# Optimization experiments

Measured on AMD Instinct MI355X. Metric: run time of the kernel, lower is better.

## Reference

```python
import jax, jax.numpy as jnp
import numpy as np

HID = 768
NSPLITS = 12
HEAD_RATIO = 2
H = NSPLITS // HEAD_RATIO          # 6 attention heads
D = HID // NSPLITS                 # 64 head size
AH = H * D                         # 384 all_head_size
KS = 9                             # conv kernel size
PAD = (KS - 1) // 2
B, S = 4, 1024


def setup_inputs() -> dict:
    key = jax.random.key(0)
    ks = jax.random.split(key, 16)
    std = 0.02
    inp = {
        "Q": jax.random.normal(ks[0], (B, S, HID), jnp.float32),
        "K": jax.random.normal(ks[1], (B, S, HID), jnp.float32),
        "V": jax.random.normal(ks[2], (B, S, HID), jnp.float32),
        "td": jax.random.uniform(ks[3], (B, S), jnp.float32),
        "mask": jax.random.randint(ks[4], (B, S), 0, 2, jnp.int32),
        # projection weights, applied as x @ W (in, out)
        "Wq": jax.random.normal(ks[5], (HID, AH), jnp.float32) * std,
        "Wk": jax.random.normal(ks[6], (HID, AH), jnp.float32) * std,
        "Wv": jax.random.normal(ks[7], (HID, AH), jnp.float32) * std,
        # separable conv: depthwise (HID, KS), pointwise (AH, HID), bias (AH,)
        "dw_w": jax.random.normal(ks[8], (HID, KS), jnp.float32) * std,
        "pw_w": jax.random.normal(ks[9], (AH, HID), jnp.float32) * std,
        "sep_b": jnp.zeros((AH,), jnp.float32),
        # conv_kernel_layer Linear(AH -> H*KS)
        "ck_W": jax.random.normal(ks[10], (AH, H * KS), jnp.float32) * std,
        "ck_b": jnp.zeros((H * KS,), jnp.float32),
        # conv_out_layer Linear(HID -> AH)
        "co_W": jax.random.normal(ks[11], (HID, AH), jnp.float32) * std,
        "co_b": jnp.zeros((AH,), jnp.float32),
        # gammas init to zeros as in torch module
        "gammas": jnp.zeros((H, 1, 1), jnp.float32),
    }
    return inp


def dist_func(scores, td, am, gammas):
    # scores: [B,H,S,S]; am: [B,1,1,S] bool key mask; entirely non-differentiable.
    s = scores.shape[-1]
    dt = scores.dtype
    amf = am.astype(dt)
    p = jax.nn.softmax(jnp.where(am, scores, -1e8), axis=-1) * amf
    distcum = jnp.cumsum(p, axis=-1)
    disttotal = jnp.sum(p, axis=-1, keepdims=True)
    # |j - i| position distance
    pos = jnp.abs(jnp.arange(s)[None, :] - jnp.arange(s)[:, None]).astype(dt)
    dist_scores = jnp.sqrt(jnp.clip((disttotal - distcum) * pos[None, None], 0.0, None))
    gamma = -jax.nn.softplus(gammas)[None]  # (1,H,1,1)
    total_effect = jnp.clip(jnp.exp(dist_scores * gamma), 1e-5, 1e5)
    # time-distance effect on strictly-lower-triangular positions
    tdn = td / jnp.maximum(jnp.linalg.norm(td, axis=-1, keepdims=True), 1e-12)
    td_scores = jnp.broadcast_to(tdn[:, None, None, :], scores.shape)
    td_sm = jax.nn.softmax(jnp.where(am, td_scores, -1e4), axis=-1)
    lower = jnp.tril(jnp.ones((s, s), dt), -1)  # (triu == 0)
    return jax.lax.stop_gradient(total_effect - td_sm * lower[None, None])


def reference(Q, K, V, td, mask, Wq, Wk, Wv, dw_w, pw_w, sep_b, ck_W, ck_b, co_W, co_b, gammas):
    b, s, hid = Q.shape
    mq = Q @ Wq  # (B,S,AH)
    mk = K @ Wk
    mv = V @ Wv
    # SeparableConv1D over sequence dim of K
    x = jnp.transpose(K, (0, 2, 1))  # (B,HID,S)
    dw = jax.lax.conv_general_dilated(
        x, dw_w[:, None, :], window_strides=(1,), padding=[(PAD, PAD)],
        feature_group_count=hid, dimension_numbers=("NCH", "OIH", "NCH"))
    pw = jnp.einsum("bcs,oc->bos", dw, pw_w) + sep_b[None, :, None]
    mkc = jnp.transpose(pw, (0, 2, 1))  # (B,S,AH)

    q = mq.reshape(b, s, H, D).transpose(0, 2, 1, 3)
    k = mk.reshape(b, s, H, D).transpose(0, 2, 1, 3)
    v = mv.reshape(b, s, H, D).transpose(0, 2, 1, 3)

    # dynamic span convolution
    conv_attn = mkc * mq                                   # (B,S,AH)
    ck = (conv_attn @ ck_W + ck_b).reshape(b, s, H, KS)
    ck = jax.nn.softmax(ck, axis=-1)                       # per-position kernel
    co = V @ co_W + co_b                                   # (B,S,AH)
    co_pad = jnp.pad(co, ((0, 0), (PAD, PAD), (0, 0)))
    idx = jnp.arange(s)[:, None] + jnp.arange(KS)[None, :]  # (S,KS)
    unf = co_pad[:, idx, :].reshape(b, s, KS, H, D)         # sliding window gather
    conv_out = jnp.einsum("bskhd,bshk->bshd", unf, ck)      # (B,S,H,D)

    # attention with distance decay
    scores = jnp.einsum("bhid,bhjd->bhij", q, k) / np.float32(np.sqrt(D))
    am = (mask[:, None, None, :] != 0)  # (B,1,1,S) key mask
    total_effect = dist_func(scores, td, am, gammas)
    scores = jnp.where(am, scores * total_effect, -1e8)
    probs = jax.nn.softmax(scores, axis=-1)
    ctx = jnp.einsum("bhij,bhjd->bhid", probs, v).transpose(0, 2, 1, 3)  # (B,S,H,D)

    out = jnp.concatenate([ctx, conv_out], axis=2).reshape(b, s, HEAD_RATIO * AH)
    return out
```

## Files before the change

### kernel.cpp

```cpp
#include <hip/hip_runtime.h>
#include <hip/hip_bf16.h>

#define HIDC 768
#define Hh   6
#define Dd   64
#define AHc  384
#define KSc  9
#define PADc 4
#define Bb   4
#define Ss   1024
#define MRr  (Bb * Ss)

typedef __attribute__((ext_vector_type(8))) __bf16 bf16x8;
typedef __attribute__((ext_vector_type(4))) __bf16 bf16x4;
typedef __attribute__((ext_vector_type(4))) float  f32x4;

__device__ __forceinline__ void gl_lds16(const void* g, void* l) {
    __builtin_amdgcn_global_load_lds(
        (const __attribute__((address_space(1))) void*)g,
        (__attribute__((address_space(3))) void*)l, 16, 0, 0);
}

__device__ __forceinline__ void split8(const float* p, bf16x8& hi, bf16x8& lo) {
    float4 x0 = *(const float4*)p;
    float4 x1 = *(const float4*)(p + 4);
    float xs[8] = {x0.x, x0.y, x0.z, x0.w, x1.x, x1.y, x1.z, x1.w};
#pragma unroll
    for (int e = 0; e < 8; ++e) {
        __bf16 hv = (__bf16)xs[e];
        hi[e] = hv;
        lo[e] = (__bf16)(xs[e] - (float)hv);
    }
}

__device__ __forceinline__ void split8r(const float* xs, bf16x8& hi, bf16x8& lo) {
#pragma unroll
    for (int e = 0; e < 8; ++e) {
        __bf16 hv = (__bf16)xs[e];
        hi[e] = hv;
        lo[e] = (__bf16)(xs[e] - (float)hv);
    }
}

__device__ __forceinline__ bf16x8 cvt8(const float* p) {
    float4 x0 = *(const float4*)p;
    float4 x1 = *(const float4*)(p + 4);
    float xs[8] = {x0.x, x0.y, x0.z, x0.w, x1.x, x1.y, x1.z, x1.w};
    bf16x8 h;
#pragma unroll
    for (int e = 0; e < 8; ++e) h[e] = (__bf16)xs[e];
    return h;
}

__global__ __launch_bounds__(256) void k_pre(
        const float* __restrict__ Wq, const float* __restrict__ Wk,
        const float* __restrict__ Wv, const float* __restrict__ coW,
        const float* __restrict__ pww, const float* __restrict__ cob,
        const float* __restrict__ sepb, const float* __restrict__ td,
        const int* __restrict__ mask, const float* __restrict__ Kin,
        const float* __restrict__ dww, const float* __restrict__ Q,
        const float* __restrict__ V,
        __bf16* __restrict__ Whi, __bf16* __restrict__ Wlo,
        float* __restrict__ biasb, float* __restrict__ td_sm,
        __bf16* __restrict__ dwbf, __bf16* __restrict__ qbf,
        __bf16* __restrict__ vbf) {
    __shared__ float shmem[64 * 65];
    int bid = blockIdx.x;
    int tid = threadIdx.x;
    if (bid < 288) {
        int z = bid / 72, rem = bid % 72;
        int n0 = (rem % 6) * 64, k0 = (rem / 6) * 64;
        const float* src = (z == 0) ? Wq : (z == 1) ? Wk : (z == 2) ? Wv : coW;
        float (*tile)[65] = (float(*)[65])shmem;
        int r = tid >> 2, cq = tid & 3;
#pragma unroll
        for (int e = 0; e < 4; ++e) {
            float4 v = *(const float4*)&src[(size_t)(k0 + r) * AHc + n0 + cq * 16 + e * 4];
            tile[r][cq * 16 + e * 4 + 0] = v.x;
            tile[r][cq * 16 + e * 4 + 1] = v.y;
            tile[r][cq * 16 + e * 4 + 2] = v.z;
            tile[r][cq * 16 + e * 4 + 3] = v.w;
        }
        __syncthreads();
        float x[16];
#pragma unroll
        for (int e = 0; e < 16; ++e) x[e] = tile[cq * 16 + e][r];
        bf16x8 h0, l0, h1, l1;
        split8r(x, h0, l0);
        split8r(x + 8, h1, l1);
        size_t dst = ((size_t)(z * AHc + n0 + r)) * HIDC + k0 + cq * 16;
        *(bf16x8*)(Whi + dst)     = h0;
        *(bf16x8*)(Whi + dst + 8) = h1;
        *(bf16x8*)(Wlo + dst)     = l0;
        *(bf16x8*)(Wlo + dst + 8) = l1;
        return;
    }
    if (bid < 432) {
        int idx = (bid - 288) * 256 + tid;
        bf16x8 hi, lo;
        split8(pww + (size_t)idx * 8, hi, lo);
        size_t dst = (size_t)4 * AHc * HIDC + (size_t)idx * 8;
        *(bf16x8*)(Whi + dst) = hi;
        *(bf16x8*)(Wlo + dst) = lo;
        return;
    }
    if (bid < 440) {
        int idx = (bid - 432) * 256 + tid;
        if (idx < 5 * AHc) {
            int z = idx / AHc, n = idx % AHc;
            biasb[idx] = (z == 3) ? cob[n] : (z == 4) ? sepb[n] : 0.f;
        }
        return;
    }
    if (bid < 444) {
        int b = bid - 440;
        float* red = shmem;
        float* tv  = shmem + 256;
        float ls = 0.f;
        for (int j = tid; j < Ss; j += 256) {
            float v = td[b * Ss + j];
            tv[j] = v;
            ls += v * v;
        }
        red[tid] = ls; __syncthreads();
        for (int s = 128; s > 0; s >>= 1) { if (tid < s) red[tid] += red[tid + s]; __syncthreads(); }
        float norm = fmaxf(sqrtf(red[0]), 1e-12f);
        __syncthreads();
        float lm = -3e38f;
        for (int j = tid; j < Ss; j += 256) {
            float v = mask[b * Ss + j] ? tv[j] / norm : -1e4f;
            tv[j] = v;
            lm = fmaxf(lm, v);
        }
        red[tid] = lm; __syncthreads();
        for (int s = 128; s > 0; s >>= 1) { if (tid < s) red[tid] = fmaxf(red[tid], red[tid + s]); __syncthreads(); }
        float m = red[0]; __syncthreads();
        float lsum = 0.f;
        for (int j = tid; j < Ss; j += 256) {
            float e = expf(tv[j] - m);
            tv[j] = e;
            lsum += e;
        }
        red[tid] = lsum; __syncthreads();
        for (int s = 128; s > 0; s >>= 1) { if (tid < s) red[tid] += red[tid + s]; __syncthreads(); }
        float inv = 1.f / red[0];
        __syncthreads();
        for (int j = tid; j < Ss; j += 256)
            td_sm[b * Ss + j] = tv[j] * inv;
        return;
    }
    int db = bid - 444;
    if (db < 3072) {
        int idx = db * 256 + tid;
        int c4 = idx % (HIDC / 4);
        int s  = (idx / (HIDC / 4)) % Ss;
        int b  = idx / ((HIDC / 4) * Ss);
        int c  = c4 * 4;
        float wv[4][KSc];
#pragma unroll
        for (int j = 0; j < 4; ++j)
#pragma unroll
            for (int k = 0; k < KSc; ++k) wv[j][k] = dww[(c + j) * KSc + k];
        float4 acc = {0.f, 0.f, 0.f, 0.f};
#pragma unroll
        for (int k = 0; k < KSc; ++k) {
            int sp = s + k - PADc;
            if (sp >= 0 && sp < Ss) {
                float4 v = *(const float4*)&Kin[(size_t)(b * Ss + sp) * HIDC + c];
                acc.x += v.x * wv[0][k]; acc.y += v.y * wv[1][k];
                acc.z += v.z * wv[2][k]; acc.w += v.w * wv[3][k];
            }
        }
        bf16x4 o = {(__bf16)acc.x, (__bf16)acc.y, (__bf16)acc.z, (__bf16)acc.w};
        *(bf16x4*)(dwbf + (size_t)idx * 4) = o;
    } else {
        const int n8 = MRr * HIDC / 8;
        int idx = (db - 3072) * 256 + tid;
        if (idx < n8) {
            *(bf16x8*)(qbf + (size_t)idx * 8) = cvt8(Q + (size_t)idx * 8);
        } else {
            int i = idx - n8;
            *(bf16x8*)(vbf + (size_t)i * 8) = cvt8(V + (size_t)i * 8);
        }
    }
}

__global__ __launch_bounds__(256) void k_gemm5(
        const __bf16* __restrict__ qbf, const float* __restrict__ Kin,
        const __bf16* __restrict__ vbf, const __bf16* __restrict__ dwbf,
        const __bf16* __restrict__ Whi, const __bf16* __restrict__ Wlo,
        const float* __restrict__ biasb, float* __restrict__ Call,
        __bf16* __restrict__ kh, __bf16* __restrict__ kl,
        __bf16* __restrict__ qh, __bf16* __restrict__ vt) {
    __shared__ __attribute__((aligned(16))) __bf16 As [128 * 32];
    __shared__ __attribute__((aligned(16))) __bf16 BsH[128 * 32];
    __shared__ __attribute__((aligned(16))) __bf16 BsL[128 * 32];

    int wg = blockIdx.x + 3 * (blockIdx.y + 32 * blockIdx.z);
    int n2 = (wg & 7) * 60 + (wg >> 3);
    int bxx = n2 % 3, byy = (n2 / 3) % 32, z = n2 / 96;

    int m0 = byy * 128, n0 = bxx * 128;
    int tid = threadIdx.x;
    int wave = tid >> 6, lane = tid & 63, quad = lane >> 4, l15 = lane & 15;

    int lrow = lane >> 2;
    int lswz = 8 * ((lane & 3) ^ (lrow & 3));

    int brow = wave * 32 + lrow;
    const __bf16* BhG0 = Whi + ((size_t)(z * AHc + n0 + brow)) * HIDC + lswz;
    const __bf16* BhG1 = BhG0 + (size_t)16 * HIDC;
    const __bf16* BlG0 = Wlo + ((size_t)(z * AHc + n0 + brow)) * HIDC + lswz;
    const __bf16* BlG1 = BlG0 + (size_t)16 * HIDC;
    __bf16* BhL0 = BsH + (wave * 2 + 0) * 512;
    __bf16* BhL1 = BsH + (wave * 2 + 1) * 512;
    __bf16* BlL0 = BsL + (wave * 2 + 0) * 512;
    __bf16* BlL1 = BsL + (wave * 2 + 1) * 512;

    const __bf16* Abf = (z == 0) ? qbf : (z == 4) ? dwbf : vbf;
    const __bf16* AG0 = Abf + ((size_t)(m0 + wave * 32 + lrow)) * HIDC + lswz;
    const __bf16* AG1 = AG0 + (size_t)16 * HIDC;
    __bf16* AL0 = As + (wave * 2 + 0) * 512;
    __bf16* AL1 = As + (wave * 2 + 1) * 512;

    int sr = tid >> 1;
    int sk = (tid & 1) * 16;
    const float* Arow = Kin + (size_t)(m0 + sr) * HIDC + sk;
    int g0 = sk >> 3;
    int d0 = sr * 32 + ((g0       ^ (sr & 3)) * 8);
    int d1 = sr * 32 + (((g0 + 1) ^ (sr & 3)) * 8);

    int swz = (quad ^ (l15 & 3)) * 8;
    f32x4 acc[4][4] = {};

    for (int k0 = 0; k0 < HIDC; k0 += 32) {
        if (z == 1) {
            const float* ap = Arow + k0;
            *(bf16x8*)&As[d0] = cvt8(ap);
            *(bf16x8*)&As[d1] = cvt8(ap + 8);
        } else {
            gl_lds16(AG0 + k0, AL0);
            gl_lds16(AG1 + k0, AL1);
        }
        gl_lds16(BhG0 + k0, BhL0);
        gl_lds16(BhG1 + k0, BhL1);
        gl_lds16(BlG0 + k0, BlL0);
        gl_lds16(BlG1 + k0, BlL1);
        __syncthreads();

        int mrow = (wave >> 1) * 64 + l15;
        int nrow = (wave & 1) * 64 + l15;
        bf16x8 ah[4], bh[4], bl[4];
#pragma unroll
        for (int mt = 0; mt < 4; ++mt)
            ah[mt] = *(bf16x8*)&As[(mrow + mt * 16) * 32 + swz];
#pragma unroll
        for (int nt = 0; nt < 4; ++nt) {
            bh[nt] = *(bf16x8*)&BsH[(nrow + nt * 16) * 32 + swz];
            bl[nt] = *(bf16x8*)&BsL[(nrow + nt * 16) * 32 + swz];
        }
#pragma unroll
        for (int mt = 0; mt < 4; ++mt)
#pragma unroll
            for (int nt = 0; nt < 4; ++nt) {
                acc[mt][nt] = __builtin_amdgcn_mfma_f32_16x16x32_bf16(ah[mt], bh[nt], acc[mt][nt], 0, 0, 0);
                acc[mt][nt] = __builtin_amdgcn_mfma_f32_16x16x32_bf16(ah[mt], bl[nt], acc[mt][nt], 0, 0, 0);
            }
        __syncthreads();
    }

    if (z == 1) {
#pragma unroll
        for (int nt = 0; nt < 4; ++nt) {
            int n = n0 + (wave & 1) * 64 + nt * 16 + l15;
#pragma unroll
            for (int mt = 0; mt < 4; ++mt) {
#pragma unroll
                for (int r = 0; r < 4; ++r) {
                    int m = m0 + (wave >> 1) * 64 + mt * 16 + quad * 4 + r;
                    float v = acc[mt][nt][r];
                    __bf16 hv = (__bf16)v;
                    kh[(size_t)m * AHc + n] = hv;
                    kl[(size_t)m * AHc + n] = (__bf16)(v - (float)hv);
                }
            }
        }
    } else if (z == 2) {
        int b = m0 >> 10;
#pragma unroll
        for (int nt = 0; nt < 4; ++nt) {
            int n = (wave & 1) * 64 + nt * 16 + l15;
            int gn = n0 + n;
            int h = gn >> 6, d = gn & 63;
#pragma unroll
            for (int mt = 0; mt < 4; ++mt) {
                int m = m0 + (wave >> 1) * 64 + mt * 16 + quad * 4;
                int s = m & (Ss - 1);
                bf16x4 o = {(__bf16)acc[mt][nt][0], (__bf16)acc[mt][nt][1],
                            (__bf16)acc[mt][nt][2], (__bf16)acc[mt][nt][3]};
                *(bf16x4*)&vt[((size_t)((b * Hh + h) * Dd + d)) * Ss + s] = o;
            }
        }
    } else if (z == 0) {
#pragma unroll
        for (int nt = 0; nt < 4; ++nt) {
            int n = n0 + (wave & 1) * 64 + nt * 16 + l15;
#pragma unroll
            for (int mt = 0; mt < 4; ++mt) {
#pragma unroll
                for (int r = 0; r < 4; ++r) {
                    int m = m0 + (wave >> 1) * 64 + mt * 16 + quad * 4 + r;
                    float v = acc[mt][nt][r];
                    Call[(size_t)m * AHc + n] = v;
                    qh[(size_t)m * AHc + n] = (__bf16)v;
                }
            }
        }
    } else {
        float* Cz = Call + (size_t)z * MRr * AHc;
        const float* bz = biasb + z * AHc;
#pragma unroll
        for (int nt = 0; nt < 4; ++nt) {
            int n = n0 + (wave & 1) * 64 + nt * 16 + l15;
            float bias = bz[n];
#pragma unroll
            for (int mt = 0; mt < 4; ++mt) {
#pragma unroll
                for (int r = 0; r < 4; ++r) {
                    int m = m0 + (wave >> 1) * 64 + mt * 16 + quad * 4 + r;
                    Cz[(size_t)m * AHc + n] = acc[mt][nt][r] + bias;
                }
            }
        }
    }
}

__global__ __launch_bounds__(256) void k_ckconv(const float* __restrict__ mkc,
                                                const float* __restrict__ mq,
                                                const float* __restrict__ ckW,
                                                const float* __restrict__ ckb,
                                                const float* __restrict__ co,
                                                float* __restrict__ out) {
    int tid = threadIdx.x;
    int lr = tid >> 6, lane = tid & 63;
    int row = blockIdx.x * 4 + lr;
    __shared__ float ca[4][AHc];
    __shared__ float ckv[4][Hh * KSc];
    for (int o = lane; o < AHc; o += 64)
        ca[lr][o] = mkc[(size_t)row * AHc + o] * mq[(size_t)row * AHc + o];
    __syncthreads();
    if (lane < Hh * KSc) {
        float acc = ckb[lane];
        for (int o = 0; o < AHc; ++o)
            acc += ca[lr][o] * ckW[o * (Hh * KSc) + lane];
        ckv[lr][lane] = acc;
    }
    __syncthreads();
    if (lane < Hh) {
        float m = -3e38f;
#pragma unroll
        for (int k = 0; k < KSc; ++k) m = fmaxf(m, ckv[lr][lane * KSc + k]);
        float e[KSc];
        float s = 0.f;
#pragma unroll
        for (int k = 0; k < KSc; ++k) { e[k] = expf(ckv[lr][lane * KSc + k] - m); s += e[k]; }
        float inv = 1.f / s;
#pragma unroll
        for (int k = 0; k < KSc; ++k) ckv[lr][lane * KSc + k] = e[k] * inv;
    }
    __syncthreads();
#pragma unroll
    for (int e = 0; e < 2; ++e) {
        int it = e * 256 + tid;
        if (it >= 4 * (AHc / 4)) break;
        int r4i = it / (AHc / 4), dq = it % (AHc / 4);
        int h = dq >> 4, d4 = dq & 15;
        int row2 = blockIdx.x * 4 + r4i;
        int s = row2 & (Ss - 1), b = row2 >> 10;
        float4 acc = {0.f, 0.f, 0.f, 0.f};
#pragma unroll
        for (int k = 0; k < KSc; ++k) {
            int sp = s + k - PADc;
            if (sp >= 0 && sp < Ss) {
                float4 v = *(const float4*)&co[(size_t)(b * Ss + sp) * AHc + h * Dd + d4 * 4];
                float wv = ckv[r4i][h * KSc + k];
                acc.x += wv * v.x; acc.y += wv * v.y; acc.z += wv * v.z; acc.w += wv * v.w;
            }
        }
        *(float4*)&out[(size_t)row2 * (2 * AHc) + AHc + h * Dd + d4 * 4] = acc;
    }
}

__device__ __forceinline__ int scix(int m, int j) {
    return m * 1024 + (j ^ (((m ^ (j >> 6)) & 7) << 2));
}

__global__ __launch_bounds__(512, 4) void k_attn(const __bf16* __restrict__ qh,
                                              const __bf16* __restrict__ kh, const __bf16* __restrict__ kl,
                                              const __bf16* __restrict__ vt,
                                              const int* __restrict__ mask,
                                              const float* __restrict__ td_sm, const float* __restrict__ gammas,
                                              float* __restrict__ out) {
    __shared__ float sc[16 * 1024];
    int wg = blockIdx.x + 64 * blockIdx.y;
    int n  = (wg & 7) * 192 + (wg >> 3);
    int bx = n & 63, by = n >> 6;
    int i0 = bx * 16;
    int h = by % Hh, b = by / Hh;
    int tid = threadIdx.x;
    int w = tid >> 6, lane = tid & 63, quad = lane >> 4, l15 = lane & 15;
    int jw = w * 128;

    bf16x8 a_hi[2];
    {
        size_t qoff = (size_t)(b * Ss + i0 + l15) * AHc + h * Dd + quad * 8;
        a_hi[0] = *(const bf16x8*)(qh + qoff);
        a_hi[1] = *(const bf16x8*)(qh + qoff + 32);
    }
#pragma unroll 4
    for (int t = 0; t < 8; ++t) {
        int jt = jw + t * 16;
        size_t koff = (size_t)(b * Ss + jt + l15) * AHc + h * Dd + quad * 8;
        f32x4 acc = {0.f, 0.f, 0.f, 0.f};
#pragma unroll
        for (int kc = 0; kc < 2; ++kc) {
            bf16x8 khv = *(const bf16x8*)(kh + koff + kc * 32);
            bf16x8 klv = *(const bf16x8*)(kl + koff + kc * 32);
            acc = __builtin_amdgcn_mfma_f32_16x16x32_bf16(a_hi[kc], khv, acc, 0, 0, 0);
            acc = __builtin_amdgcn_mfma_f32_16x16x32_bf16(a_hi[kc], klv, acc, 0, 0, 0);
        }
#pragma unroll
        for (int r = 0; r < 4; ++r)
            sc[scix(quad * 4 + r, jt + l15)] = acc[r] * 0.125f;
    }
    __syncthreads();

    const int* mrow = mask + b * Ss;
    const float* tdrow = td_sm + b * Ss;
    float gamma = -log1pf(expf(gammas[h]));
    int jb = lane << 4;
    __attribute__((aligned(16))) int marr[16];
    {
        const int4* mp = (const int4*)(mrow + jb);
#pragma unroll
        for (int k = 0; k < 4; ++k) ((int4*)marr)[k] = mp[k];
    }
    __attribute__((aligned(16))) float tdv[16];
    {
        const float4* tp = (const float4*)(tdrow + jb);
#pragma unroll
        for (int k = 0; k < 4; ++k) ((float4*)tdv)[k] = tp[k];
    }

    {
        int mA = w * 2, mB = mA + 1;
        int iA = i0 + mA, iB = i0 + mB;
        __attribute__((aligned(16))) float sA[16], sB[16];
        float pA[16], pB[16];
#pragma unroll
        for (int g = 0; g < 4; ++g) {
            *(f32x4*)(sA + 4 * g) = *(const f32x4*)&sc[scix(mA, jb + 4 * g)];
            *(f32x4*)(sB + 4 * g) = *(const f32x4*)&sc[scix(mB, jb + 4 * g)];
        }
        float mxA = -1e30f, mxB = -1e30f;
#pragma unroll
        for (int jj = 0; jj < 16; ++jj) {
            mxA = fmaxf(mxA, marr[jj] ? sA[jj] : -1e30f);
            mxB = fmaxf(mxB, marr[jj] ? sB[jj] : -1e30f);
        }
#pragma unroll
        for (int d = 1; d < 64; d <<= 1) {
            mxA = fmaxf(mxA, __shfl_xor(mxA, d));
            mxB = fmaxf(mxB, __shfl_xor(mxB, d));
        }
#pragma unroll
        for (int jj = 0; jj < 16; ++jj) {
            pA[jj] = marr[jj] ? __expf(sA[jj] - mxA) : 0.f;
            pB[jj] = marr[jj] ? __expf(sB[jj] - mxB) : 0.f;
        }
#pragma unroll
        for (int jj = 1; jj < 16; ++jj) { pA[jj] += pA[jj - 1]; pB[jj] += pB[jj - 1]; }
        float tA = pA[15], tB = pB[15];
        float incA = tA, incB = tB;
#pragma unroll
        for (int dlt = 1; dlt < 64; dlt <<= 1) {
            float vA = __shfl_up(incA, dlt);
            float vB = __shfl_up(incB, dlt);
            if (lane >= dlt) { incA += vA; incB += vB; }
        }
        float offA = incA - tA, offB = incB - tB;
        float totA = __shfl(incA, 63), totB = __shfl(incB, 63);
        float invA = 1.f / fmaxf(totA, 1e-30f), invB = 1.f / fmaxf(totB, 1e-30f);
        float mx2A = -1e30f, mx2B = -1e30f;
#pragma unroll
        for (int jj = 0; jj < 16; ++jj) {
            int j = jb + jj;
            float cumA = pA[jj] + offA, cumB = pB[jj] + offB;
            float posA = fabsf((float)(j - iA));
            float posB = fabsf((float)(j - iB));
            float dsA = sqrtf(fmaxf((totA - cumA) * invA * posA, 0.f));
            float dsB = sqrtf(fmaxf((totB - cumB) * invB * posB, 0.f));
            float teA = fminf(fmaxf(__expf(dsA * gamma), 1e-5f), 1e5f);
            float teB = fminf(fmaxf(__expf(dsB * gamma), 1e-5f), 1e5f);
            float tdj = tdv[jj];
            float multA = teA - ((j < iA) ? tdj : 0.f);
            float multB = teB - ((j < iB) ? tdj : 0.f);
            float s2A = marr[jj] ? sA[jj] * multA : -1e8f;
            float s2B = marr[jj] ? sB[jj] * multB : -1e8f;
            sA[jj] = s2A; sB[jj] = s2B;
            mx2A = fmaxf(mx2A, s2A); mx2B = fmaxf(mx2B, s2B);
        }
#pragma unroll
        for (int d = 1; d < 64; d <<= 1) {
            mx2A = fmaxf(mx2A, __shfl_xor(mx2A, d));
            mx2B = fmaxf(mx2B, __shfl_xor(mx2B, d));
        }
        float smA = 0.f, smB = 0.f;
#pragma unroll
        for (int jj = 0; jj < 16; ++jj) {
            sA[jj] = __expf(sA[jj] - mx2A); smA += sA[jj];
            sB[jj] = __expf(sB[jj] - mx2B); smB += sB[jj];
        }
#pragma unroll
        for (int d = 1; d < 64; d <<= 1) {
            smA += __shfl_xor(smA, d);
            smB += __shfl_xor(smB, d);
        }
        float i2A = 1.f / smA, i2B = 1.f / smB;
#pragma unroll
        for (int jj = 0; jj < 16; ++jj) { sA[jj] *= i2A; sB[jj] *= i2B; }
#pragma unroll
        for (int g = 0; g < 4; ++g) {
            *(f32x4*)&sc[scix(mA, jb + 4 * g)] = *(const f32x4*)(sA + 4 * g);
            *(f32x4*)&sc[scix(mB, jb + 4 * g)] = *(const f32x4*)(sB + 4 * g);
        }
    }
    __syncthreads();

    f32x4 oacc[4] = {};
    const __bf16* vtb = vt + (size_t)(b * Hh + h) * Dd * Ss;
#pragma unroll
    for (int kc = 0; kc < 4; ++kc) {
        int j0 = jw + kc * 32 + quad * 8;
        __attribute__((aligned(16))) float x[8];
        *(f32x4*)x       = *(const f32x4*)&sc[scix(l15, j0)];
        *(f32x4*)(x + 4) = *(const f32x4*)&sc[scix(l15, j0 + 4)];
        bf16x8 p_hi, p_lo;
        split8r(x, p_hi, p_lo);
#pragma unroll
        for (int nt = 0; nt < 4; ++nt) {
            int d = nt * 16 + l15;
            bf16x8 vv = *(const bf16x8*)(vtb + (size_t)d * Ss + j0);
            oacc[nt] = __builtin_amdgcn_mfma_f32_16x16x32_bf16(p_hi, vv, oacc[nt], 0, 0, 0);
            oacc[nt] = __builtin_amdgcn_mfma_f32_16x16x32_bf16(p_lo, vv, oacc[nt], 0, 0, 0);
        }
    }
    __syncthreads();
#pragma unroll
    for (int nt = 0; nt < 4; ++nt)
#pragma unroll
        for (int r = 0; r < 4; ++r)
            sc[w * 1024 + (quad * 4 + r) * 64 + nt * 16 + l15] = oacc[nt][r];
    __syncthreads();
#pragma unroll
    for (int e = 0; e < 2; ++e) {
        int idx = e * 512 + tid;
        int m = idx >> 6, dd = idx & 63;
        float v = 0.f;
#pragma unroll
        for (int ww = 0; ww < 8; ++ww) v += sc[ww * 1024 + idx];
        out[(size_t)(b * Ss + i0 + m) * (2 * AHc) + h * Dd + dd] = v;
    }
}

extern "C" void kernel_launch(void* const* d_in, const int* in_sizes, int n_in,
                              void* d_out, int out_size, void* d_ws, size_t ws_size,
                              hipStream_t stream) {
    const float* Q    = (const float*)d_in[0];
    const float* Kin  = (const float*)d_in[1];
    const float* V    = (const float*)d_in[2];
    const float* td   = (const float*)d_in[3];
    const int*   mask = (const int*)d_in[4];
    const float* Wq   = (const float*)d_in[5];
    const float* Wk   = (const float*)d_in[6];
    const float* Wv   = (const float*)d_in[7];
    const float* dww  = (const float*)d_in[8];
    const float* pww  = (const float*)d_in[9];
    const float* sepb = (const float*)d_in[10];
    const float* ckW  = (const float*)d_in[11];
    const float* ckb  = (const float*)d_in[12];
    const float* coW  = (const float*)d_in[13];
    const float* cob  = (const float*)d_in[14];
    const float* gam  = (const float*)d_in[15];
    float* out = (float*)d_out;
    float* ws = (float*)d_ws;

    float* mq    = ws;
    float* mks   = mq    + (size_t)MRr * AHc;
    float* mvs   = mks   + (size_t)MRr * AHc;
    float* co    = mvs   + (size_t)MRr * AHc;
    float* mkc   = co    + (size_t)MRr * AHc;
    float* dwr   = mkc   + (size_t)MRr * AHc;
    float* tdsm  = dwr   + (size_t)MRr * HIDC;
    float* biasb = tdsm  + (size_t)Bb * Ss;

    __bf16* dwbf = (__bf16*)dwr;
    __bf16* qbf  = (__bf16*)(dwr + (size_t)MRr * HIDC / 2);
    __bf16* kh = (__bf16*)mks;
    __bf16* kl = kh + (size_t)MRr * AHc;
    __bf16* vt = (__bf16*)mvs;
    __bf16* qh = vt + (size_t)MRr * AHc;

    __bf16* Whi = (__bf16*)d_out;
    __bf16* Wlo = Whi + (size_t)5 * AHc * HIDC;
    __bf16* vbf = Wlo + (size_t)5 * AHc * HIDC;

    k_pre<<<6588, 256, 0, stream>>>(Wq, Wk, Wv, coW, pww, cob, sepb, td, mask,
                                    Kin, dww, Q, V, Whi, Wlo, biasb, tdsm,
                                    dwbf, qbf, vbf);

    dim3 gg(AHc / 128, MRr / 128, 5);
    k_gemm5<<<gg, 256, 0, stream>>>(qbf, Kin, vbf, dwbf, Whi, Wlo, biasb, mq, kh, kl, qh, vt);

    k_ckconv<<<MRr / 4, 256, 0, stream>>>(mkc, mq, ckW, ckb, co, out);

    dim3 ga(Ss / 16, Bb * Hh);
    k_attn<<<ga, 512, 0, stream>>>(qh, kh, kl, vt, mask, tdsm, gam, out);
}
```

Measured before the change: 272.6 us.

## Double-buffer GEMM LDS tiles, pack attention mask bits, tweak ckconv and attn bounds

The projection GEMM now keeps two LDS tile buffers and issues the global-to-LDS loads for the next K slice before computing the current one, so load latency can overlap the MFMA work. In the attention kernel the per-lane mask is packed into a 16-bit integer rather than a 16-int array, and masked scores are set to a sentinel before the max and exp steps. This is meant to cut register pressure and the number of selects. The ckconv inner loop gets an unrolled strided weight pointer, and the attention launch bounds are given as explicit AMDGPU attributes. Doubling the GEMM's LDS use may reduce occupancy, and exp of the -1e30 sentinel must underflow to zero to keep the masked probabilities correct.

```diff
diff --git a/kernel.cpp b/kernel.cpp
--- a/kernel.cpp
+++ b/kernel.cpp
@@ -192,9 +192,9 @@
         const float* __restrict__ biasb, float* __restrict__ Call,
         __bf16* __restrict__ kh, __bf16* __restrict__ kl,
         __bf16* __restrict__ qh, __bf16* __restrict__ vt) {
-    __shared__ __attribute__((aligned(16))) __bf16 As [128 * 32];
-    __shared__ __attribute__((aligned(16))) __bf16 BsH[128 * 32];
-    __shared__ __attribute__((aligned(16))) __bf16 BsL[128 * 32];
+    __shared__ __attribute__((aligned(16))) __bf16 As [2][128 * 32];
+    __shared__ __attribute__((aligned(16))) __bf16 BsH[2][128 * 32];
+    __shared__ __attribute__((aligned(16))) __bf16 BsL[2][128 * 32];
 
     int wg = blockIdx.x + 3 * (blockIdx.y + 32 * blockIdx.z);
     int n2 = (wg & 7) * 60 + (wg >> 3);
@@ -206,22 +206,19 @@
 
     int lrow = lane >> 2;
     int lswz = 8 * ((lane & 3) ^ (lrow & 3));
+
+    int off0 = (wave * 2 + 0) * 512;
+    int off1 = (wave * 2 + 1) * 512;
 
     int brow = wave * 32 + lrow;
     const __bf16* BhG0 = Whi + ((size_t)(z * AHc + n0 + brow)) * HIDC + lswz;
     const __bf16* BhG1 = BhG0 + (size_t)16 * HIDC;
     const __bf16* BlG0 = Wlo + ((size_t)(z * AHc + n0 + brow)) * HIDC + lswz;
     const __bf16* BlG1 = BlG0 + (size_t)16 * HIDC;
-    __bf16* BhL0 = BsH + (wave * 2 + 0) * 512;
-    __bf16* BhL1 = BsH + (wave * 2 + 1) * 512;
-    __bf16* BlL0 = BsL + (wave * 2 + 0) * 512;
-    __bf16* BlL1 = BsL + (wave * 2 + 1) * 512;
 
     const __bf16* Abf = (z == 0) ? qbf : (z == 4) ? dwbf : vbf;
     const __bf16* AG0 = Abf + ((size_t)(m0 + wave * 32 + lrow)) * HIDC + lswz;
     const __bf16* AG1 = AG0 + (size_t)16 * HIDC;
-    __bf16* AL0 = As + (wave * 2 + 0) * 512;
-    __bf16* AL1 = As + (wave * 2 + 1) * 512;
 
     int sr = tid >> 1;
     int sk = (tid & 1) * 16;
@@ -231,33 +228,50 @@
     int d1 = sr * 32 + (((g0 + 1) ^ (sr & 3)) * 8);
 
     int swz = (quad ^ (l15 & 3)) * 8;
+    int mrow = (wave >> 1) * 64 + l15;
+    int nrow = (wave & 1) * 64 + l15;
     f32x4 acc[4][4] = {};
 
-    for (int k0 = 0; k0 < HIDC; k0 += 32) {
-        if (z == 1) {
-            const float* ap = Arow + k0;
-            *(bf16x8*)&As[d0] = cvt8(ap);
-            *(bf16x8*)&As[d1] = cvt8(ap + 8);
-        } else {
-            gl_lds16(AG0 + k0, AL0);
-            gl_lds16(AG1 + k0, AL1);
-        }
-        gl_lds16(BhG0 + k0, BhL0);
-        gl_lds16(BhG1 + k0, BhL1);
-        gl_lds16(BlG0 + k0, BlL0);
-        gl_lds16(BlG1 + k0, BlL1);
-        __syncthreads();
-
-        int mrow = (wave >> 1) * 64 + l15;
-        int nrow = (wave & 1) * 64 + l15;
+    if (z == 1) {
+        *(bf16x8*)&As[0][d0] = cvt8(Arow);
+        *(bf16x8*)&As[0][d1] = cvt8(Arow + 8);
+    } else {
+        gl_lds16(AG0, &As[0][off0]);
+        gl_lds16(AG1, &As[0][off1]);
+    }
+    gl_lds16(BhG0, &BsH[0][off0]);
+    gl_lds16(BhG1, &BsH[0][off1]);
+    gl_lds16(BlG0, &BsL[0][off0]);
+    gl_lds16(BlG1, &BsL[0][off1]);
+    __syncthreads();
+
+    int cur = 0;
+    for (int t = 0; t < HIDC / 32; ++t) {
+        int nxt = cur ^ 1;
+        if (t + 1 < HIDC / 32) {
+            int k1 = (t + 1) * 32;
+            if (z == 1) {
+                const float* ap = Arow + k1;
+                *(bf16x8*)&As[nxt][d0] = cvt8(ap);
+                *(bf16x8*)&As[nxt][d1] = cvt8(ap + 8);
+            } else {
+                gl_lds16(AG0 + k1, &As[nxt][off0]);
+                gl_lds16(AG1 + k1, &As[nxt][off1]);
+            }
+            gl_lds16(BhG0 + k1, &BsH[nxt][off0]);
+            gl_lds16(BhG1 + k1, &BsH[nxt][off1]);
+            gl_lds16(BlG0 + k1, &BsL[nxt][off0]);
+            gl_lds16(BlG1 + k1, &BsL[nxt][off1]);
+        }
+
         bf16x8 ah[4], bh[4], bl[4];
 #pragma unroll
         for (int mt = 0; mt < 4; ++mt)
-            ah[mt] = *(bf16x8*)&As[(mrow + mt * 16) * 32 + swz];
+            ah[mt] = *(bf16x8*)&As[cur][(mrow + mt * 16) * 32 + swz];
 #pragma unroll
         for (int nt = 0; nt < 4; ++nt) {
-            bh[nt] = *(bf16x8*)&BsH[(nrow + nt * 16) * 32 + swz];
-            bl[nt] = *(bf16x8*)&BsL[(nrow + nt * 16) * 32 + swz];
+            bh[nt] = *(bf16x8*)&BsH[cur][(nrow + nt * 16) * 32 + swz];
+            bl[nt] = *(bf16x8*)&BsL[cur][(nrow + nt * 16) * 32 + swz];
         }
 #pragma unroll
         for (int mt = 0; mt < 4; ++mt)
@@ -267,6 +281,7 @@
                 acc[mt][nt] = __builtin_amdgcn_mfma_f32_16x16x32_bf16(ah[mt], bl[nt], acc[mt][nt], 0, 0, 0);
             }
         __syncthreads();
+        cur = nxt;
     }
 
     if (z == 1) {
@@ -351,8 +366,10 @@
     __syncthreads();
     if (lane < Hh * KSc) {
         float acc = ckb[lane];
+        const float* wp = ckW + lane;
+#pragma unroll 8
         for (int o = 0; o < AHc; ++o)
-            acc += ca[lr][o] * ckW[o * (Hh * KSc) + lane];
+            acc += ca[lr][o] * wp[o * (Hh * KSc)];
         ckv[lr][lane] = acc;
     }
     __syncthreads();
@@ -395,12 +412,13 @@
     return m * 1024 + (j ^ (((m ^ (j >> 6)) & 7) << 2));
 }
 
-__global__ __launch_bounds__(512, 4) void k_attn(const __bf16* __restrict__ qh,
-                                              const __bf16* __restrict__ kh, const __bf16* __restrict__ kl,
-                                              const __bf16* __restrict__ vt,
-                                              const int* __restrict__ mask,
-                                              const float* __restrict__ td_sm, const float* __restrict__ gammas,
-                                              float* __restrict__ out) {
+__global__ __attribute__((amdgpu_flat_work_group_size(512, 512), amdgpu_waves_per_eu(4, 4)))
+void k_attn(const __bf16* __restrict__ qh,
+            const __bf16* __restrict__ kh, const __bf16* __restrict__ kl,
+            const __bf16* __restrict__ vt,
+            const int* __restrict__ mask,
+            const float* __restrict__ td_sm, const float* __restrict__ gammas,
+            float* __restrict__ out) {
     __shared__ float sc[16 * 1024];
     int wg = blockIdx.x + 64 * blockIdx.y;
     int n  = (wg & 7) * 192 + (wg >> 3);
@@ -435,15 +453,20 @@
     }
     __syncthreads();
 
-    const int* mrow = mask + b * Ss;
     const float* tdrow = td_sm + b * Ss;
     float gamma = -log1pf(expf(gammas[h]));
     int jb = lane << 4;
-    __attribute__((aligned(16))) int marr[16];
+    int mbits = 0;
     {
-        const int4* mp = (const int4*)(mrow + jb);
-#pragma unroll
-        for (int k = 0; k < 4; ++k) ((int4*)marr)[k] = mp[k];
+        const int4* mp = (const int4*)(mask + b * Ss + jb);
+#pragma unroll
+        for (int k = 0; k < 4; ++k) {
+            int4 mv = mp[k];
+            mbits |= (mv.x != 0) << (4 * k + 0);
+            mbits |= (mv.y != 0) << (4 * k + 1);
+            mbits |= (mv.z != 0) << (4 * k + 2);
+            mbits |= (mv.w != 0) << (4 * k + 3);
+        }
     }
     __attribute__((aligned(16))) float tdv[16];
     {
@@ -462,11 +485,15 @@
             *(f32x4*)(sA + 4 * g) = *(const f32x4*)&sc[scix(mA, jb + 4 * g)];
             *(f32x4*)(sB + 4 * g) = *(const f32x4*)&sc[scix(mB, jb + 4 * g)];
         }
+#pragma unroll
+        for (int jj = 0; jj < 16; ++jj) {
+            if (!((mbits >> jj) & 1)) { sA[jj] = -1e30f; sB[jj] = -1e30f; }
+        }
         float mxA = -1e30f, mxB = -1e30f;
 #pragma unroll
         for (int jj = 0; jj < 16; ++jj) {
-            mxA = fmaxf(mxA, marr[jj] ? sA[jj] : -1e30f);
-            mxB = fmaxf(mxB, marr[jj] ? sB[jj] : -1e30f);
+            mxA = fmaxf(mxA, sA[jj]);
+            mxB = fmaxf(mxB, sB[jj]);
         }
 #pragma unroll
         for (int d = 1; d < 64; d <<= 1) {
@@ -475,8 +502,8 @@
         }
 #pragma unroll
         for (int jj = 0; jj < 16; ++jj) {
-            pA[jj] = marr[jj] ? __expf(sA[jj] - mxA) : 0.f;
-            pB[jj] = marr[jj] ? __expf(sB[jj] - mxB) : 0.f;
+            pA[jj] = __expf(sA[jj] - mxA);
+            pB[jj] = __expf(sB[jj] - mxB);
         }
 #pragma unroll
         for (int jj = 1; jj < 16; ++jj) { pA[jj] += pA[jj - 1]; pB[jj] += pB[jj - 1]; }
@@ -495,6 +522,7 @@
 #pragma unroll
         for (int jj = 0; jj < 16; ++jj) {
             int j = jb + jj;
+            int bit = (mbits >> jj) & 1;
             float cumA = pA[jj] + offA, cumB = pB[jj] + offB;
             float posA = fabsf((float)(j - iA));
             float posB = fabsf((float)(j - iB));
@@ -505,8 +533,8 @@
             float tdj = tdv[jj];
             float multA = teA - ((j < iA) ? tdj : 0.f);
             float multB = teB - ((j < iB) ? tdj : 0.f);
-            float s2A = marr[jj] ? sA[jj] * multA : -1e8f;
-            float s2B = marr[jj] ? sB[jj] * multB : -1e8f;
+            float s2A = bit ? sA[jj] * multA : -1e8f;
+            float s2B = bit ? sB[jj] * multB : -1e8f;
             sA[jj] = s2A; sB[jj] = s2B;
             mx2A = fmaxf(mx2A, s2A); mx2B = fmaxf(mx2B, s2B);
         }
```

After: 278.8 us. 2.3% more time.

## Drop low-part weight split in projection GEMM and pack attention mask bits

Applied to the files above, without the earlier changes.

The projection GEMM's weights now use only the bf16 high part, with no hi/lo split-precision correction. That removes half the weight loads, LDS traffic and MFMA instructions, and k_pre no longer writes the Wlo buffer. Separately, the attention kernel packs the key mask into a bitfield and pre-masks scores to simplify the softmax, k_ckconv's small dot loop is unrolled, and the launch attributes move to amdgpu_waves_per_eu. Dropping the weight low part reduces accuracy of the projections, which feed the attention scores and the distance-decay computation.

```diff
diff --git a/kernel.cpp b/kernel.cpp
--- a/kernel.cpp
+++ b/kernel.cpp
@@ -21,18 +21,6 @@
         (__attribute__((address_space(3))) void*)l, 16, 0, 0);
 }
 
-__device__ __forceinline__ void split8(const float* p, bf16x8& hi, bf16x8& lo) {
-    float4 x0 = *(const float4*)p;
-    float4 x1 = *(const float4*)(p + 4);
-    float xs[8] = {x0.x, x0.y, x0.z, x0.w, x1.x, x1.y, x1.z, x1.w};
-#pragma unroll
-    for (int e = 0; e < 8; ++e) {
-        __bf16 hv = (__bf16)xs[e];
-        hi[e] = hv;
-        lo[e] = (__bf16)(xs[e] - (float)hv);
-    }
-}
-
 __device__ __forceinline__ void split8r(const float* xs, bf16x8& hi, bf16x8& lo) {
 #pragma unroll
     for (int e = 0; e < 8; ++e) {
@@ -60,7 +48,7 @@
         const int* __restrict__ mask, const float* __restrict__ Kin,
         const float* __restrict__ dww, const float* __restrict__ Q,
         const float* __restrict__ V,
-        __bf16* __restrict__ Whi, __bf16* __restrict__ Wlo,
+        __bf16* __restrict__ Whi,
         float* __restrict__ biasb, float* __restrict__ td_sm,
         __bf16* __restrict__ dwbf, __bf16* __restrict__ qbf,
         __bf16* __restrict__ vbf) {
@@ -85,23 +73,18 @@
         float x[16];
 #pragma unroll
         for (int e = 0; e < 16; ++e) x[e] = tile[cq * 16 + e][r];
-        bf16x8 h0, l0, h1, l1;
-        split8r(x, h0, l0);
-        split8r(x + 8, h1, l1);
+        bf16x8 h0, h1;
+#pragma unroll
+        for (int e = 0; e < 8; ++e) { h0[e] = (__bf16)x[e]; h1[e] = (__bf16)x[8 + e]; }
         size_t dst = ((size_t)(z * AHc + n0 + r)) * HIDC + k0 + cq * 16;
         *(bf16x8*)(Whi + dst)     = h0;
         *(bf16x8*)(Whi + dst + 8) = h1;
-        *(bf16x8*)(Wlo + dst)     = l0;
-        *(bf16x8*)(Wlo + dst + 8) = l1;
         return;
     }
     if (bid < 432) {
         int idx = (bid - 288) * 256 + tid;
-        bf16x8 hi, lo;
-        split8(pww + (size_t)idx * 8, hi, lo);
         size_t dst = (size_t)4 * AHc * HIDC + (size_t)idx * 8;
-        *(bf16x8*)(Whi + dst) = hi;
-        *(bf16x8*)(Wlo + dst) = lo;
+        *(bf16x8*)(Whi + dst) = cvt8(pww + (size_t)idx * 8);
         return;
     }
     if (bid < 440) {
@@ -188,13 +171,12 @@
 __global__ __launch_bounds__(256) void k_gemm5(
         const __bf16* __restrict__ qbf, const float* __restrict__ Kin,
         const __bf16* __restrict__ vbf, const __bf16* __restrict__ dwbf,
-        const __bf16* __restrict__ Whi, const __bf16* __restrict__ Wlo,
+        const __bf16* __restrict__ Whi,
         const float* __restrict__ biasb, float* __restrict__ Call,
         __bf16* __restrict__ kh, __bf16* __restrict__ kl,
         __bf16* __restrict__ qh, __bf16* __restrict__ vt) {
     __shared__ __attribute__((aligned(16))) __bf16 As [128 * 32];
     __shared__ __attribute__((aligned(16))) __bf16 BsH[128 * 32];
-    __shared__ __attribute__((aligned(16))) __bf16 BsL[128 * 32];
 
     int wg = blockIdx.x + 3 * (blockIdx.y + 32 * blockIdx.z);
     int n2 = (wg & 7) * 60 + (wg >> 3);
@@ -210,12 +192,8 @@
     int brow = wave * 32 + lrow;
     const __bf16* BhG0 = Whi + ((size_t)(z * AHc + n0 + brow)) * HIDC + lswz;
     const __bf16* BhG1 = BhG0 + (size_t)16 * HIDC;
-    const __bf16* BlG0 = Wlo + ((size_t)(z * AHc + n0 + brow)) * HIDC + lswz;
-    const __bf16* BlG1 = BlG0 + (size_t)16 * HIDC;
     __bf16* BhL0 = BsH + (wave * 2 + 0) * 512;
     __bf16* BhL1 = BsH + (wave * 2 + 1) * 512;
-    __bf16* BlL0 = BsL + (wave * 2 + 0) * 512;
-    __bf16* BlL1 = BsL + (wave * 2 + 1) * 512;
 
     const __bf16* Abf = (z == 0) ? qbf : (z == 4) ? dwbf : vbf;
     const __bf16* AG0 = Abf + ((size_t)(m0 + wave * 32 + lrow)) * HIDC + lswz;
@@ -244,28 +222,22 @@
         }
         gl_lds16(BhG0 + k0, BhL0);
         gl_lds16(BhG1 + k0, BhL1);
-        gl_lds16(BlG0 + k0, BlL0);
-        gl_lds16(BlG1 + k0, BlL1);
         __syncthreads();
 
         int mrow = (wave >> 1) * 64 + l15;
         int nrow = (wave & 1) * 64 + l15;
-        bf16x8 ah[4], bh[4], bl[4];
+        bf16x8 ah[4], bh[4];
 #pragma unroll
         for (int mt = 0; mt < 4; ++mt)
             ah[mt] = *(bf16x8*)&As[(mrow + mt * 16) * 32 + swz];
 #pragma unroll
-        for (int nt = 0; nt < 4; ++nt) {
+        for (int nt = 0; nt < 4; ++nt)
             bh[nt] = *(bf16x8*)&BsH[(nrow + nt * 16) * 32 + swz];
-            bl[nt] = *(bf16x8*)&BsL[(nrow + nt * 16) * 32 + swz];
-        }
 #pragma unroll
         for (int mt = 0; mt < 4; ++mt)
 #pragma unroll
-            for (int nt = 0; nt < 4; ++nt) {
+            for (int nt = 0; nt < 4; ++nt)
                 acc[mt][nt] = __builtin_amdgcn_mfma_f32_16x16x32_bf16(ah[mt], bh[nt], acc[mt][nt], 0, 0, 0);
-                acc[mt][nt] = __builtin_amdgcn_mfma_f32_16x16x32_bf16(ah[mt], bl[nt], acc[mt][nt], 0, 0, 0);
-            }
         __syncthreads();
     }
 
@@ -351,8 +323,10 @@
     __syncthreads();
     if (lane < Hh * KSc) {
         float acc = ckb[lane];
+        const float* wp = ckW + lane;
+#pragma unroll 8
         for (int o = 0; o < AHc; ++o)
-            acc += ca[lr][o] * ckW[o * (Hh * KSc) + lane];
+            acc += ca[lr][o] * wp[o * (Hh * KSc)];
         ckv[lr][lane] = acc;
     }
     __syncthreads();
@@ -395,12 +369,13 @@
     return m * 1024 + (j ^ (((m ^ (j >> 6)) & 7) << 2));
 }
 
-__global__ __launch_bounds__(512, 4) void k_attn(const __bf16* __restrict__ qh,
-                                              const __bf16* __restrict__ kh, const __bf16* __restrict__ kl,
-                                              const __bf16* __restrict__ vt,
-                                              const int* __restrict__ mask,
-                                              const float* __restrict__ td_sm, const float* __restrict__ gammas,
-                                              float* __restrict__ out) {
+__global__ __attribute__((amdgpu_flat_work_group_size(512, 512), amdgpu_waves_per_eu(4, 4)))
+void k_attn(const __bf16* __restrict__ qh,
+            const __bf16* __restrict__ kh, const __bf16* __restrict__ kl,
+            const __bf16* __restrict__ vt,
+            const int* __restrict__ mask,
+            const float* __restrict__ td_sm, const float* __restrict__ gammas,
+            float* __restrict__ out) {
     __shared__ float sc[16 * 1024];
     int wg = blockIdx.x + 64 * blockIdx.y;
     int n  = (wg & 7) * 192 + (wg >> 3);
@@ -435,15 +410,20 @@
     }
     __syncthreads();
 
-    const int* mrow = mask + b * Ss;
     const float* tdrow = td_sm + b * Ss;
     float gamma = -log1pf(expf(gammas[h]));
     int jb = lane << 4;
-    __attribute__((aligned(16))) int marr[16];
+    int mbits = 0;
     {
-        const int4* mp = (const int4*)(mrow + jb);
-#pragma unroll
-        for (int k = 0; k < 4; ++k) ((int4*)marr)[k] = mp[k];
+        const int4* mp = (const int4*)(mask + b * Ss + jb);
+#pragma unroll
+        for (int k = 0; k < 4; ++k) {
+            int4 mv = mp[k];
+            mbits |= (mv.x != 0) << (4 * k + 0);
+            mbits |= (mv.y != 0) << (4 * k + 1);
+            mbits |= (mv.z != 0) << (4 * k + 2);
+            mbits |= (mv.w != 0) << (4 * k + 3);
+        }
     }
     __attribute__((aligned(16))) float tdv[16];
     {
@@ -462,11 +442,15 @@
             *(f32x4*)(sA + 4 * g) = *(const f32x4*)&sc[scix(mA, jb + 4 * g)];
             *(f32x4*)(sB + 4 * g) = *(const f32x4*)&sc[scix(mB, jb + 4 * g)];
         }
+#pragma unroll
+        for (int jj = 0; jj < 16; ++jj) {
+            if (!((mbits >> jj) & 1)) { sA[jj] = -1e30f; sB[jj] = -1e30f; }
+        }
         float mxA = -1e30f, mxB = -1e30f;
 #pragma unroll
         for (int jj = 0; jj < 16; ++jj) {
-            mxA = fmaxf(mxA, marr[jj] ? sA[jj] : -1e30f);
-            mxB = fmaxf(mxB, marr[jj] ? sB[jj] : -1e30f);
+            mxA = fmaxf(mxA, sA[jj]);
+            mxB = fmaxf(mxB, sB[jj]);
         }
 #pragma unroll
         for (int d = 1; d < 64; d <<= 1) {
@@ -475,8 +459,8 @@
         }
 #pragma unroll
         for (int jj = 0; jj < 16; ++jj) {
-            pA[jj] = marr[jj] ? __expf(sA[jj] - mxA) : 0.f;
-            pB[jj] = marr[jj] ? __expf(sB[jj] - mxB) : 0.f;
+            pA[jj] = __expf(sA[jj] - mxA);
+            pB[jj] = __expf(sB[jj] - mxB);
         }
 #pragma unroll
         for (int jj = 1; jj < 16; ++jj) { pA[jj] += pA[jj - 1]; pB[jj] += pB[jj - 1]; }
@@ -495,6 +479,7 @@
 #pragma unroll
         for (int jj = 0; jj < 16; ++jj) {
             int j = jb + jj;
+            int bit = (mbits >> jj) & 1;
             float cumA = pA[jj] + offA, cumB = pB[jj] + offB;
             float posA = fabsf((float)(j - iA));
             float posB = fabsf((float)(j - iB));
@@ -505,8 +490,8 @@
             float tdj = tdv[jj];
             float multA = teA - ((j < iA) ? tdj : 0.f);
             float multB = teB - ((j < iB) ? tdj : 0.f);
-            float s2A = marr[jj] ? sA[jj] * multA : -1e8f;
-            float s2B = marr[jj] ? sB[jj] * multB : -1e8f;
+            float s2A = bit ? sA[jj] * multA : -1e8f;
+            float s2B = bit ? sB[jj] * multB : -1e8f;
             sA[jj] = s2A; sB[jj] = s2B;
             mx2A = fmaxf(mx2A, s2A); mx2B = fmaxf(mx2B, s2B);
         }
@@ -612,18 +597,17 @@
     __bf16* qh = vt + (size_t)MRr * AHc;
 
     __bf16* Whi = (__bf16*)d_out;
-    __bf16* Wlo = Whi + (size_t)5 * AHc * HIDC;
-    __bf16* vbf = Wlo + (size_t)5 * AHc * HIDC;
+    __bf16* vbf = Whi + (size_t)5 * AHc * HIDC;
 
     k_pre<<<6588, 256, 0, stream>>>(Wq, Wk, Wv, coW, pww, cob, sepb, td, mask,
-                                    Kin, dww, Q, V, Whi, Wlo, biasb, tdsm,
+                                    Kin, dww, Q, V, Whi, biasb, tdsm,
                                     dwbf, qbf, vbf);
 
     dim3 gg(AHc / 128, MRr / 128, 5);
-    k_gemm5<<<gg, 256, 0, stream>>>(qbf, Kin, vbf, dwbf, Whi, Wlo, biasb, mq, kh, kl, qh, vt);
+    k_gemm5<<<gg, 256, 0, stream>>>(qbf, Kin, vbf, dwbf, Whi, biasb, mq, kh, kl, qh, vt);
 
     k_ckconv<<<MRr / 4, 256, 0, stream>>>(mkc, mq, ckW, ckb, co, out);
 
-    dim3 ga(Ss / 16, Bb * Hh);
+    dim3 ga(64, 24);
     k_attn<<<ga, 512, 0, stream>>>(qh, kh, kl, vt, mask, tdsm, gam, out);
 }
```

Measured after the change: 268.3 us, median of 2. About the same (-1.6%).
